# Kernel optimization log

Measured on AMD Instinct MI355X. Metric: run time of the kernel, lower is better.

The kernel has to match this reference:

```python
import jax, jax.numpy as jnp
import numpy as np
import math

E = 256          # embed_dims
H = 8            # num_heads
ITER = 2         # iterative steps
PC_RANGE = (-140.8, -40.0, -3.0, 140.8, 40.0, 1.0)


def sine_embed(pos, num_feats):
    # pos: (..., 3) in (0,1); returns (..., 3*num_feats), per-coord interleaved sin/cos
    scale = 2.0 * math.pi
    i = jnp.arange(num_feats, dtype=jnp.float32)
    dim_t = 10000.0 ** (2.0 * jnp.floor(i / 2.0) / num_feats)
    p = pos[..., None] * scale / dim_t                      # (..., 3, F)
    emb = jnp.stack([jnp.sin(p[..., 0::2]), jnp.cos(p[..., 1::2])], axis=-1)
    emb = emb.reshape(p.shape[:-1] + (num_feats,))          # (..., 3, F)
    return emb.reshape(pos.shape[:-1] + (3 * num_feats,))


def mha(q, k, v, Wi, bi, Wo, bo, n_heads):
    # torch nn.MultiheadAttention math, seq-first layout: q (L,N,C), k/v (M,N,C)
    L, N, C = q.shape
    D = C // n_heads
    qp = (q @ Wi[:C].T + bi[:C]).reshape(L, N, n_heads, D)
    kp = (k @ Wi[C:2 * C].T + bi[C:2 * C]).reshape(k.shape[0], N, n_heads, D)
    vp = (v @ Wi[2 * C:].T + bi[2 * C:]).reshape(v.shape[0], N, n_heads, D)
    scores = jnp.einsum('lnhd,mnhd->nhlm', qp, kp) / math.sqrt(D)
    attn = jax.nn.softmax(scores, axis=-1)
    o = jnp.einsum('nhlm,mnhd->lnhd', attn, vp).reshape(L, N, C)
    return o @ Wo.T + bo


def setup_inputs() -> dict:
    key = jax.random.key(0)
    ks = jax.random.split(key, 12)
    Q, TOT, B, LMAX = 2048, 40, 8, 5
    s = 0.02
    return {
        'x': jax.random.normal(ks[0], (Q, TOT, E), jnp.float32),
        'reference_points': jax.random.uniform(ks[1], (TOT, Q, 3), jnp.float32),
        'pairwise_t_matrix': jax.random.normal(ks[2], (B, LMAX, LMAX, 4, 4), jnp.float32),
        'record_len': np.full((B,), 5, dtype=np.int64),
        'in_proj_w': jax.random.normal(ks[3], (3 * E, E), jnp.float32) * s,
        'in_proj_b': jnp.zeros((3 * E,), jnp.float32),
        'out_w': jax.random.normal(ks[4], (E, E), jnp.float32) * s,
        'out_b': jnp.zeros((E,), jnp.float32),
        'bev_w1': jax.random.normal(ks[5], (E, 3 * E), jnp.float32) * s,
        'bev_b1': jnp.zeros((E,), jnp.float32),
        'bev_w2': jax.random.normal(ks[6], (E, E), jnp.float32) * s,
        'bev_b2': jnp.zeros((E,), jnp.float32),
    }


def reference(x, reference_points, pairwise_t_matrix, in_proj_w, in_proj_b,
              out_w, out_b, bev_w1, bev_b1, bev_w2, bev_b2, record_len):
    rl = np.asarray(record_len)
    offsets = np.concatenate([[0], np.cumsum(rl)]).astype(int)
    lo = jnp.asarray(PC_RANGE[:3], jnp.float32)
    hi = jnp.asarray(PC_RANGE[3:], jnp.float32)

    x_cav = jnp.transpose(x, (1, 0, 2))                    # (total_cav, Q, C)
    ref = reference_points * (hi - lo) + lo                # un-normalize to pc_range

    outs = []
    for b in range(len(rl)):
        s, e = offsets[b], offsets[b + 1]
        n = e - s
        b_x = x_cav[s:e]                                   # (n, Q, C)
        if n == 1:
            outs.append(b_x)
            continue
        b_ref = ref[s:e]                                   # (n, Q, 3)
        t_ego = pairwise_t_matrix[b, :n, 0]                # (n, 4, 4) transform-to-ego
        homo = jnp.concatenate([b_ref, jnp.ones(b_ref.shape[:-1] + (1,), b_ref.dtype)], axis=-1)
        trans = jax.nn.sigmoid(jnp.einsum('nij,nqj->nqi', t_ego, homo)[..., :3])
        pe = sine_embed(trans, E)                          # (n, Q, 3E)
        bev = jax.nn.relu(pe @ bev_w1.T + bev_b1) @ bev_w2.T + bev_b2  # (n, Q, C)

        ego = b_x[0:1]
        neigh = b_x[1:]                                    # (n-1, Q, C)
        kk = neigh + bev[1:]
        for _ in range(ITER):
            q = jnp.broadcast_to(ego, neigh.shape)
            o = q + mha(q, kk, neigh, in_proj_w, in_proj_b, out_w, out_b, H)
            ego = jnp.sum(o, axis=0, keepdims=True)
        outs.append(jnp.concatenate([ego, neigh], axis=0))

    out = jnp.concatenate(outs, axis=0)                    # (total_cav, Q, C)
    return jnp.transpose(out, (1, 0, 2))                   # (Q, total_cav, C)
```

## Files before the change

kernel.cpp:

```cpp
#include <hip/hip_runtime.h>
#include <cstdint>
#include <cstddef>

typedef __bf16 bf16;
typedef __attribute__((ext_vector_type(8))) __bf16 bf16x8;
typedef __attribute__((ext_vector_type(4))) float f32x4;
typedef __attribute__((ext_vector_type(4))) unsigned int u32x4;

#define QN 2048

#if __has_builtin(__builtin_amdgcn_sinf)
#define SIN_REV(x) __builtin_amdgcn_sinf(x)
#define COS_REV(x) __builtin_amdgcn_cosf(x)
#else
#define SIN_REV(x) __sinf((x) * 6.283185307179586f)
#define COS_REV(x) __cosf((x) * 6.283185307179586f)
#endif

__device__ __forceinline__ float sigmoidf_(float v) { return 1.0f / (1.0f + __expf(-v)); }

__device__ __forceinline__ bf16x8 cvt8(const float* p) {
  const f32x4* p4 = (const f32x4*)p;
  f32x4 lo = p4[0], hi = p4[1];
  bf16x8 r;
#pragma unroll
  for (int j = 0; j < 4; ++j) { r[j] = (bf16)lo[j]; r[j + 4] = (bf16)hi[j]; }
  return r;
}

__device__ __forceinline__ void load_lds16(const bf16* g, bf16* l) {
  __builtin_amdgcn_global_load_lds(
      (const __attribute__((address_space(1))) void*)g,
      (__attribute__((address_space(3))) void*)l, 16, 0, 0);
}

__global__ __launch_bounds__(256) void copy_ker(const u32x4* __restrict__ in,
                                                u32x4* __restrict__ out, int n) {
  int i = blockIdx.x * 256 + threadIdx.x;
  if (i >= n) return;
  int t = (i >> 6) % 40;
  if ((t % 5) == 0) return;
  out[i] = in[i];
}

__global__ __launch_bounds__(256) void cvtw_ker(const float* __restrict__ ipw,
                                                const float* __restrict__ ow,
                                                const float* __restrict__ w1,
                                                bf16* __restrict__ wb) {
  int e = (blockIdx.x * 256 + threadIdx.x) * 8;
  const float* src; int off;
  if (e < 196608)      { src = ipw; off = e; }
  else if (e < 262144) { src = ow;  off = e - 196608; }
  else                 { src = w1;  off = e - 262144; }
  *(bf16x8*)(wb + e) = cvt8(src + off);
}

__global__ __launch_bounds__(256) void wcomb_ker(const float* __restrict__ ipw,
                                                 const float* __restrict__ ipb,
                                                 const float* __restrict__ w2f,
                                                 const float* __restrict__ b2f,
                                                 bf16* __restrict__ Wc,
                                                 float* __restrict__ bkf) {
  __shared__ float row[256];
  __shared__ float red[256];
  const int j = blockIdx.x, l = threadIdx.x;
  row[l] = ipw[65536 + j * 256 + l];
  __syncthreads();
  float acc = 0.f;
#pragma unroll 4
  for (int m = 0; m < 256; ++m) acc += row[m] * w2f[m * 256 + l];
  Wc[(size_t)j * 512 + l] = (bf16)acc;
  Wc[(size_t)j * 512 + 256 + l] = (bf16)row[l];
  red[l] = row[l] * b2f[l];
  __syncthreads();
  for (int s = 128; s > 0; s >>= 1) {
    if (l < s) red[l] += red[l + s];
    __syncthreads();
  }
  if (l == 0) bkf[j] = ipb[256 + j] + red[0];
}

__global__ __launch_bounds__(256) void pe_gemm_ker(
    const bf16* __restrict__ W, const float* __restrict__ bias,
    const float* __restrict__ rp, const float* __restrict__ pm,
    bf16* __restrict__ outB) {
  const int tid = threadIdx.x;
  const int bidm = blockIdx.x >> 1;
  const int bidn = blockIdx.x & 1;
  const int rowBase = bidm << 7;
  const int colBase = bidn << 7;
  const int wave = tid >> 6, lane = tid & 63;
  const int m16 = lane & 15, quad = lane >> 4;
  const int wr = wave >> 1, wc = wave & 1;

  float tr[3][4];
#pragma unroll
  for (int mt = 0; mt < 4; ++mt) {
    int r = rowBase + (wr << 6) + (mt << 4) + m16;
    int b = r >> 13, j = (r >> 11) & 3, q = r & 2047;
    int t = b * 5 + 1 + j;
    const float* rpp = rp + ((size_t)t * QN + q) * 3;
    float r0 = rpp[0] * 281.6f - 140.8f;
    float r1 = rpp[1] * 80.0f - 40.0f;
    float r2 = rpp[2] * 4.0f - 3.0f;
    const float* T = pm + (size_t)t * 80;
    tr[0][mt] = sigmoidf_(T[0] * r0 + T[1] * r1 + T[2] * r2 + T[3]);
    tr[1][mt] = sigmoidf_(T[4] * r0 + T[5] * r1 + T[6] * r2 + T[7]);
    tr[2][mt] = sigmoidf_(T[8] * r0 + T[9] * r1 + T[10] * r2 + T[11]);
  }

  const bf16* bsrc = W + (size_t)(colBase + (wc << 6) + m16) * 768 + (quad << 3);

  const float freq0 = exp2f((float)(quad << 2) * -0.10381025296522975f);
  const float R = 0.9305720409296979f;
  const float R16 = 0.31622776601683794f;

  f32x4 acc[4][4] = {};

#pragma unroll
  for (int c = 0; c < 3; ++c) {
    float fq = freq0;
#pragma unroll
    for (int s = 0; s < 8; ++s) {
      const int k0 = (c << 8) + (s << 5);
      bf16x8 bfr[4];
#pragma unroll
      for (int nt = 0; nt < 4; ++nt)
        bfr[nt] = *(const bf16x8*)(bsrc + (size_t)(nt << 4) * 768 + k0);
      const float f0 = fq, f1 = f0 * R, f2 = f1 * R, f3 = f2 * R;
      bf16x8 afr[4];
#pragma unroll
      for (int mt = 0; mt < 4; ++mt) {
        const float tc = tr[c][mt];
        const float a0 = tc * f0, a1 = tc * f1, a2 = tc * f2, a3 = tc * f3;
        afr[mt][0] = (bf16)SIN_REV(a0); afr[mt][1] = (bf16)COS_REV(a0);
        afr[mt][2] = (bf16)SIN_REV(a1); afr[mt][3] = (bf16)COS_REV(a1);
        afr[mt][4] = (bf16)SIN_REV(a2); afr[mt][5] = (bf16)COS_REV(a2);
        afr[mt][6] = (bf16)SIN_REV(a3); afr[mt][7] = (bf16)COS_REV(a3);
      }
#pragma unroll
      for (int mt = 0; mt < 4; ++mt)
#pragma unroll
        for (int nt = 0; nt < 4; ++nt)
          acc[mt][nt] = __builtin_amdgcn_mfma_f32_16x16x32_bf16(
              afr[mt], bfr[nt], acc[mt][nt], 0, 0, 0);
      fq = f3 * R * R16 / R16;
      fq = f0 * R16;
    }
  }

#pragma unroll
  for (int mt = 0; mt < 4; ++mt) {
#pragma unroll
    for (int nt = 0; nt < 4; ++nt) {
      const int col = colBase + (wc << 6) + (nt << 4) + m16;
      const float bv = bias[col];
#pragma unroll
      for (int rg = 0; rg < 4; ++rg) {
        const int r = rowBase + (wr << 6) + (mt << 4) + (quad << 2) + rg;
        float v = acc[mt][nt][rg] + bv;
        outB[(size_t)r * 256 + col] = (bf16)fmaxf(v, 0.0f);
      }
    }
  }
}

template <int AMODE, int EPI, int KDIM>
__global__ __launch_bounds__(256) void gemm_ker(
    const bf16* __restrict__ A, const float* __restrict__ Af,
    const bf16* __restrict__ W, const float* __restrict__ bias,
    const float* __restrict__ x, const float* __restrict__ rp,
    const float* __restrict__ pm, const float* __restrict__ egoPrev,
    bf16* __restrict__ outB, float* __restrict__ outF) {
  __shared__ bf16 As[128][40];
  __shared__ bf16 Bs[128][32];

  const int tid = threadIdx.x;
  const int bidm = blockIdx.x >> 1;
  const int bidn = blockIdx.x & 1;
  const int rowBase = bidm << 7;
  const int colBase = bidn << 7;

  const int wave = tid >> 6, lane = tid & 63;
  const int m16 = lane & 15, quad = lane >> 4;
  const int wr = wave >> 1, wc = wave & 1;

  const int sRow = tid >> 1, sHalf = tid & 1;
  const int rgA = rowBase + sRow;

  const float* afp = nullptr;
  if constexpr (AMODE == 2 || AMODE == 5) {
    int b = rgA >> 13, j = (rgA >> 11) & 3, q = rgA & 2047;
    afp = x + (((size_t)q * 40 + b * 5 + 1 + j) << 8);
  } else if constexpr (AMODE == 3) {
    int b = rgA >> 11, q = rgA & 2047;
    afp = x + (((size_t)q * 40 + b * 5) << 8);
  } else if constexpr (AMODE == 4) {
    afp = Af + (size_t)rgA * 256;
  }

  const bf16* wsrc = W + (size_t)(colBase + (wave << 5) + (lane >> 2)) * KDIM + ((lane & 3) << 3);
  bf16* bdst0 = &Bs[(wave << 5)][0];
  bf16* bdst1 = &Bs[(wave << 5) + 16][0];

  f32x4 acc[4][4] = {};

  for (int k0 = 0; k0 < KDIM; k0 += 32) {
    load_lds16(wsrc + k0, bdst0);
    load_lds16(wsrc + (size_t)16 * KDIM + k0, bdst1);

    bf16x8 a0, a1;
    if constexpr (AMODE == 0) {
      const bf16* ap = A + (size_t)rgA * KDIM + k0 + (sHalf << 4);
      a0 = ((const bf16x8*)ap)[0];
      a1 = ((const bf16x8*)ap)[1];
    } else if constexpr (AMODE == 5) {
      if (k0 < 256) {
        const bf16* ap = A + ((size_t)rgA << 8) + k0 + (sHalf << 4);
        a0 = ((const bf16x8*)ap)[0];
        a1 = ((const bf16x8*)ap)[1];
      } else {
        const float* fp = afp + (k0 - 256) + (sHalf << 4);
        a0 = cvt8(fp);
        a1 = cvt8(fp + 8);
      }
    } else {
      const float* fp = afp + k0 + (sHalf << 4);
      a0 = cvt8(fp);
      a1 = cvt8(fp + 8);
    }
    *(bf16x8*)(&As[sRow][sHalf << 4]) = a0;
    *(bf16x8*)(&As[sRow][(sHalf << 4) + 8]) = a1;
    __syncthreads();

    bf16x8 afr[4], bfr[4];
#pragma unroll
    for (int mt = 0; mt < 4; ++mt)
      afr[mt] = *(const bf16x8*)(&As[(wr << 6) + (mt << 4) + m16][quad << 3]);
#pragma unroll
    for (int nt = 0; nt < 4; ++nt)
      bfr[nt] = *(const bf16x8*)(&Bs[(wc << 6) + (nt << 4) + m16][quad << 3]);
#pragma unroll
    for (int mt = 0; mt < 4; ++mt)
#pragma unroll
      for (int nt = 0; nt < 4; ++nt)
        acc[mt][nt] = __builtin_amdgcn_mfma_f32_16x16x32_bf16(
            afr[mt], bfr[nt], acc[mt][nt], 0, 0, 0);
    __syncthreads();
  }

#pragma unroll
  for (int mt = 0; mt < 4; ++mt) {
#pragma unroll
    for (int nt = 0; nt < 4; ++nt) {
      const int col = colBase + (wc << 6) + (nt << 4) + m16;
      const float bv = bias[col];
#pragma unroll
      for (int rg = 0; rg < 4; ++rg) {
        const int r = rowBase + (wr << 6) + (mt << 4) + (quad << 2) + rg;
        float v = acc[mt][nt][rg] + bv;
        if constexpr (EPI == 0) {
          outB[(size_t)r * 256 + col] = (bf16)fmaxf(v, 0.0f);
        } else if constexpr (EPI == 2) {
          outB[(size_t)r * 256 + col] = (bf16)v;
        } else if constexpr (EPI == 3) {
          int b = r >> 11, q = r & 2047;
          float xe = x[(((size_t)q * 40 + b * 5) << 8) + col];
          outF[(size_t)r * 256 + col] = 4.0f * (xe + v);
        } else if constexpr (EPI == 4) {
          int b = r >> 11, q = r & 2047;
          float e1 = egoPrev[(size_t)r * 256 + col];
          outF[(((size_t)q * 40 + b * 5) << 8) + col] = 4.0f * (e1 + v);
        }
      }
    }
  }
}

__global__ __launch_bounds__(256) void attn_ker(const bf16* __restrict__ qp,
                                                const bf16* __restrict__ kp,
                                                const bf16* __restrict__ vp,
                                                bf16* __restrict__ o) {
  int p = blockIdx.x * 256 + threadIdx.x;
  int h = p & 7;
  int re = p >> 3;
  int b = re >> 11;
  int q = re & 2047;
  const bf16x8* qpv = (const bf16x8*)(qp + ((size_t)re << 8) + h * 32);
  float qv[32];
#pragma unroll
  for (int i = 0; i < 4; ++i) {
    bf16x8 t = qpv[i];
#pragma unroll
    for (int j = 0; j < 8; ++j) qv[i * 8 + j] = (float)t[j];
  }
  size_t base = ((size_t)(b * 4) * QN + q) * 256 + h * 32;
  float s[4];
#pragma unroll
  for (int m = 0; m < 4; ++m) {
    const bf16x8* kv = (const bf16x8*)(kp + base + (size_t)m * (QN * 256));
    float a = 0.f;
#pragma unroll
    for (int i = 0; i < 4; ++i) {
      bf16x8 t = kv[i];
#pragma unroll
      for (int j = 0; j < 8; ++j) a += qv[i * 8 + j] * (float)t[j];
    }
    s[m] = a * 0.17677669529663687f;
  }
  float mx = fmaxf(fmaxf(s[0], s[1]), fmaxf(s[2], s[3]));
  float e0 = __expf(s[0] - mx), e1 = __expf(s[1] - mx);
  float e2 = __expf(s[2] - mx), e3 = __expf(s[3] - mx);
  float inv = 1.0f / (e0 + e1 + e2 + e3);
  float w[4] = {e0 * inv, e1 * inv, e2 * inv, e3 * inv};
  float ov[32] = {};
#pragma unroll
  for (int m = 0; m < 4; ++m) {
    const bf16x8* vv = (const bf16x8*)(vp + base + (size_t)m * (QN * 256));
#pragma unroll
    for (int i = 0; i < 4; ++i) {
      bf16x8 t = vv[i];
#pragma unroll
      for (int j = 0; j < 8; ++j) ov[i * 8 + j] += w[m] * (float)t[j];
    }
  }
  bf16x8* op = (bf16x8*)(o + ((size_t)re << 8) + h * 32);
#pragma unroll
  for (int i = 0; i < 4; ++i) {
    bf16x8 t;
#pragma unroll
    for (int j = 0; j < 8; ++j) t[j] = (bf16)ov[i * 8 + j];
    op[i] = t;
  }
}

extern "C" void kernel_launch(void* const* d_in, const int* in_sizes, int n_in,
                              void* d_out, int out_size, void* d_ws, size_t ws_size,
                              hipStream_t stream) {
  (void)n_in; (void)out_size; (void)ws_size;
  const float* x   = (const float*)d_in[0];
  const float* rp  = (const float*)d_in[1];
  const float* pm  = (const float*)d_in[2];
  const int wbase = (in_sizes[3] == 8) ? 4 : 3;
  const float* ipw = (const float*)d_in[wbase + 0];
  const float* ipb = (const float*)d_in[wbase + 1];
  const float* ow  = (const float*)d_in[wbase + 2];
  const float* obv = (const float*)d_in[wbase + 3];
  const float* w1  = (const float*)d_in[wbase + 4];
  const float* b1  = (const float*)d_in[wbase + 5];
  const float* w2  = (const float*)d_in[wbase + 6];
  const float* b2  = (const float*)d_in[wbase + 7];
  float* out = (float*)d_out;
  char* ws = (char*)d_ws;

  bf16* h    = (bf16*)(ws + 0);
  bf16* qp   = (bf16*)(ws + 0);
  bf16* oo   = (bf16*)(ws + 8388608);
  bf16* kp   = (bf16*)(ws + 33554432);
  bf16* vp   = (bf16*)(ws + 67108864);
  float* egoF = (float*)(ws + 100663296);
  bf16* wb   = (bf16*)(ws + 117440512);
  bf16* Wc   = (bf16*)(ws + 118489088);
  float* bkf = (float*)(ws + 118751232);
  const bf16* wq  = wb;
  const bf16* wv  = wb + 131072;
  const bf16* owb = wb + 196608;
  const bf16* w1b = wb + 262144;

  cvtw_ker<<<224, 256, 0, stream>>>(ipw, ow, w1, wb);
  wcomb_ker<<<256, 256, 0, stream>>>(ipw, ipb, w2, b2, Wc, bkf);
  copy_ker<<<20480, 256, 0, stream>>>((const u32x4*)x, (u32x4*)out, 5242880);
  pe_gemm_ker<<<1024, 256, 0, stream>>>(w1b, b1, rp, pm, h);
  gemm_ker<5, 2, 512><<<1024, 256, 0, stream>>>(h, nullptr, Wc, bkf, x, rp, pm, nullptr, kp, nullptr);
  gemm_ker<2, 2, 256><<<1024, 256, 0, stream>>>(nullptr, nullptr, wv, ipb + 512, x, rp, pm, nullptr, vp, nullptr);
  gemm_ker<3, 2, 256><<<256, 256, 0, stream>>>(nullptr, nullptr, wq, ipb, x, rp, pm, nullptr, qp, nullptr);
  attn_ker<<<512, 256, 0, stream>>>(qp, kp, vp, oo);
  gemm_ker<0, 3, 256><<<256, 256, 0, stream>>>(oo, nullptr, owb, obv, x, rp, pm, nullptr, nullptr, egoF);
  gemm_ker<4, 2, 256><<<256, 256, 0, stream>>>(nullptr, egoF, wq, ipb, x, rp, pm, nullptr, qp, nullptr);
  attn_ker<<<512, 256, 0, stream>>>(qp, kp, vp, oo);
  gemm_ker<0, 4, 256><<<256, 256, 0, stream>>>(oo, nullptr, owb, obv, x, rp, pm, egoF, nullptr, out);
}
```

Baseline: 414.7 us.

## Stage PE GEMM weight tiles through double-buffered swizzled LDS

The PE-embedding GEMM used to load its B fragments straight from global memory in every k-step. It now copies 128x128 bf16 weight tiles into a double-buffered shared-memory array with an XOR swizzle and prefetches the next tile while computing the current one. The frequency stepping is restructured per 128-wide tile. This targets global-load latency and redundant weight reads, at the cost of 64KB of LDS per block, which may limit occupancy.

New measurement: 391.2 us. -5.7%, faster.

```diff
diff --git a/kernel.cpp b/kernel.cpp
--- a/kernel.cpp
+++ b/kernel.cpp
@@ -84,6 +84,8 @@
     const bf16* __restrict__ W, const float* __restrict__ bias,
     const float* __restrict__ rp, const float* __restrict__ pm,
     bf16* __restrict__ outB) {
+  __shared__ bf16 Bs[2][128][128];
+
   const int tid = threadIdx.x;
   const int bidm = blockIdx.x >> 1;
   const int bidn = blockIdx.x & 1;
@@ -92,6 +94,7 @@
   const int wave = tid >> 6, lane = tid & 63;
   const int m16 = lane & 15, quad = lane >> 4;
   const int wr = wave >> 1, wc = wave & 1;
+  const int cg = lane >> 4, b16 = lane & 15;
 
   float tr[3][4];
 #pragma unroll
@@ -109,25 +112,41 @@
     tr[2][mt] = sigmoidf_(T[8] * r0 + T[9] * r1 + T[10] * r2 + T[11]);
   }
 
-  const bf16* bsrc = W + (size_t)(colBase + (wc << 6) + m16) * 768 + (quad << 3);
-
-  const float freq0 = exp2f((float)(quad << 2) * -0.10381025296522975f);
+  const float fA = exp2f((float)(quad << 2) * -0.10381025296522975f);
   const float R = 0.9305720409296979f;
   const float R16 = 0.31622776601683794f;
 
+#define PE_STAGE(P, T)                                                        \
+  {                                                                           \
+    _Pragma("unroll") for (int i = 0; i < 8; ++i) {                           \
+      int col = (wave << 5) + (i << 2) + cg;                                  \
+      const bf16* src = W + (size_t)(colBase + col) * 768 + ((T) << 7) +      \
+                        ((b16 ^ (col & 7)) << 3);                             \
+      load_lds16(src, &Bs[(P)][(wave << 5) + (i << 2)][0]);                   \
+    }                                                                         \
+  }
+
   f32x4 acc[4][4] = {};
 
-#pragma unroll
-  for (int c = 0; c < 3; ++c) {
-    float fq = freq0;
-#pragma unroll
-    for (int s = 0; s < 8; ++s) {
-      const int k0 = (c << 8) + (s << 5);
+  PE_STAGE(0, 0);
+  __syncthreads();
+
+#pragma unroll
+  for (int t = 0; t < 6; ++t) {
+    const int p = t & 1;
+    if (t < 5) PE_STAGE(p ^ 1, t + 1);
+    const int c = t >> 1;
+    float fstep = fA * ((t & 1) ? 0.01f : 1.0f);
+#pragma unroll
+    for (int kk = 0; kk < 4; ++kk) {
       bf16x8 bfr[4];
 #pragma unroll
-      for (int nt = 0; nt < 4; ++nt)
-        bfr[nt] = *(const bf16x8*)(bsrc + (size_t)(nt << 4) * 768 + k0);
-      const float f0 = fq, f1 = f0 * R, f2 = f1 * R, f3 = f2 * R;
+      for (int nt = 0; nt < 4; ++nt) {
+        int col = (wc << 6) + (nt << 4) + m16;
+        bfr[nt] = *(const bf16x8*)(
+            &Bs[p][col][((kk << 5) + (quad << 3)) ^ ((col & 7) << 3)]);
+      }
+      const float f0 = fstep, f1 = f0 * R, f2 = f1 * R, f3 = f2 * R;
       bf16x8 afr[4];
 #pragma unroll
       for (int mt = 0; mt < 4; ++mt) {
@@ -144,10 +163,11 @@
         for (int nt = 0; nt < 4; ++nt)
           acc[mt][nt] = __builtin_amdgcn_mfma_f32_16x16x32_bf16(
               afr[mt], bfr[nt], acc[mt][nt], 0, 0, 0);
-      fq = f3 * R * R16 / R16;
-      fq = f0 * R16;
-    }
-  }
+      fstep *= R16;
+    }
+    __syncthreads();
+  }
+#undef PE_STAGE
 
 #pragma unroll
   for (int mt = 0; mt < 4; ++mt) {
```
